# Kernel optimization log

Measured on AMD Instinct MI355X. Metric: run time of the kernel, lower is better.

Reference implementation:

```python
import jax, jax.numpy as jnp
import numpy as np

B, M_IN, N_OUT = 131072, 64, 64


def setup_inputs() -> dict:
    key = jax.random.key(0)
    k1, k2, k3 = jax.random.split(key, 3)
    x = jax.random.normal(k1, (B, M_IN, 4), dtype=jnp.float32)
    x = x.at[:, :, 0].set(0.0)  # pure quaternion input (w-component = 0)
    stdv_w = (2.0 / (M_IN + N_OUT)) ** 0.5
    W_q = jax.random.normal(k2, (N_OUT, M_IN, 4), dtype=jnp.float32) * (stdv_w / 2.0)
    theta_q = jax.random.normal(k3, (N_OUT, 4), dtype=jnp.float32) * 0.01
    theta_q = theta_q.at[:, 0].set(0.0)  # pure quaternion threshold
    return {"x_batch": x, "W_q": W_q, "theta_q": theta_q}


def _hamilton_sum(x, W):
    """s[b,n] = sum_m W[n,m] (x) x[b,m]  (Hamilton product, W on the left).
    x: (B, M, 4), W: (N, M, 4) -> (B, N, 4)"""
    ww, wx, wy, wz = (W[..., i] for i in range(4))   # each (N, M)
    xw, xx, xy, xz = (x[..., i] for i in range(4))   # each (B, M)
    dot = lambda p, q: jnp.einsum('bm,nm->bn', p, q)
    sw = dot(xw, ww) - dot(xx, wx) - dot(xy, wy) - dot(xz, wz)
    sx = dot(xx, ww) + dot(xw, wx) + dot(xz, wy) - dot(xy, wz)
    sy = dot(xy, ww) - dot(xz, wx) + dot(xw, wy) + dot(xx, wz)
    sz = dot(xz, ww) + dot(xy, wx) - dot(xx, wy) + dot(xw, wz)
    return jnp.stack([sw, sx, sy, sz], axis=-1)


def reference(x_batch, W_q, theta_q):
    # Isokawa quaternion neuron: s = sum_m W (x) x - theta; y = sigmoid(s) per component.
    s = _hamilton_sum(x_batch, W_q) - theta_q[None, :, :]  # (B, N, 4) pre-activation (s_internal)
    return jax.nn.sigmoid(s)
```

## Files before the change

### kernel.cpp

```cpp
#include <hip/hip_runtime.h>
#include <hip/hip_bf16.h>


typedef __bf16 bf16_t;
typedef bf16_t bf16x8 __attribute__((ext_vector_type(8)));
typedef bf16_t bf16x4v __attribute__((ext_vector_type(4)));
typedef float f32x4 __attribute__((ext_vector_type(4)));

#define B_TOTAL 131072
#define KDIM 256
#define NDIM 256
#define ROWS 64
#define THREADS 512
#define LDS_STRIDE 264

__global__ void coef_kernel(const float* __restrict__ W, bf16_t* __restrict__ coef) {
    const int widx[4][4] = {{0,1,2,3},{1,0,3,2},{2,3,0,1},{3,2,1,0}};
    const float sgn[4][4] = {{1.f,-1.f,-1.f,-1.f},
                             {1.f, 1.f,-1.f, 1.f},
                             {1.f, 1.f, 1.f,-1.f},
                             {1.f,-1.f, 1.f, 1.f}};
    int F = blockIdx.x * blockDim.x + threadIdx.x;
    int j    = F & 7;
    int lane = (F >> 3) & 63;
    int ks   = (F >> 9) & 7;
    int nt   = F >> 12;
    int col  = nt * 16 + (lane & 15);
    int k    = ks * 32 + (lane >> 4) * 8 + j;
    int n = col >> 2, oc = col & 3;
    int m = k >> 2,   ic = k & 3;
    coef[F] = (bf16_t)(sgn[oc][ic] * W[n * 256 + m * 4 + widx[oc][ic]]);
}

__global__ __launch_bounds__(THREADS, 4)
void main_kernel(const float* __restrict__ x, const bf16x8* __restrict__ coef,
                 const float* __restrict__ theta, float* __restrict__ out) {
    __shared__ __align__(16) bf16_t xs[ROWS * LDS_STRIDE];

    const int tid  = threadIdx.x;
    const int row0 = blockIdx.x * ROWS;
    const int wave = tid >> 6, lane = tid & 63;
    const int l15  = lane & 15, quad = lane >> 4;

    const float4* xp = (const float4*)(x + (long)row0 * KDIM);
    float4 v[8];
#pragma unroll
    for (int i = 0; i < 8; i++) v[i] = xp[tid + THREADS * i];

    bf16x8 breg[2][8];
#pragma unroll
    for (int ct = 0; ct < 2; ct++)
#pragma unroll
        for (int ks = 0; ks < 8; ks++)
            breg[ct][ks] = coef[((wave * 2 + ct) * 8 + ks) * 64 + lane];

#pragma unroll
    for (int i = 0; i < 8; i++) {
        int f = tid + THREADS * i;
        int r = f >> 6;
        int c = (f & 63) * 4;
        bf16x4v w;
        w.x = (bf16_t)v[i].x; w.y = (bf16_t)v[i].y;
        w.z = (bf16_t)v[i].z; w.w = (bf16_t)v[i].w;
        *(bf16x4v*)&xs[r * LDS_STRIDE + c] = w;
    }
    __syncthreads();

    f32x4 acc[4][2];
#pragma unroll
    for (int rt = 0; rt < 4; rt++)
#pragma unroll
        for (int ct = 0; ct < 2; ct++) acc[rt][ct] = (f32x4)(0.f);

#pragma unroll
    for (int ks = 0; ks < 8; ks++) {
        bf16x8 a[4];
#pragma unroll
        for (int rt = 0; rt < 4; rt++)
            a[rt] = *(const bf16x8*)&xs[(rt * 16 + l15) * LDS_STRIDE + ks * 32 + quad * 8];
#pragma unroll
        for (int rt = 0; rt < 4; rt++)
#pragma unroll
            for (int ct = 0; ct < 2; ct++)
                acc[rt][ct] = __builtin_amdgcn_mfma_f32_16x16x32_bf16(
                    a[rt], breg[ct][ks], acc[rt][ct], 0, 0, 0);
    }

    float th[2];
#pragma unroll
    for (int ct = 0; ct < 2; ct++) th[ct] = theta[wave * 32 + ct * 16 + l15];

#pragma unroll
    for (int rt = 0; rt < 4; rt++) {
        int rbase = row0 + rt * 16 + quad * 4;
#pragma unroll
        for (int ct = 0; ct < 2; ct++) {
            int col = wave * 32 + ct * 16 + l15;
#pragma unroll
            for (int r = 0; r < 4; r++) {
                float s = acc[rt][ct][r] - th[ct];
                float y = 1.0f / (1.0f + __expf(-s));
                out[(long)(rbase + r) * NDIM + col] = y;
            }
        }
    }
}

extern "C" void kernel_launch(void* const* d_in, const int* in_sizes, int n_in,
                              void* d_out, int out_size, void* d_ws, size_t ws_size,
                              hipStream_t stream) {
    const float* x     = (const float*)d_in[0];
    const float* W     = (const float*)d_in[1];
    const float* theta = (const float*)d_in[2];
    float* out = (float*)d_out;
    bf16_t* coef = (bf16_t*)d_ws;

    if (ws_size < 65536 * sizeof(bf16_t)) return;

    coef_kernel<<<256, 256, 0, stream>>>(W, coef);
    main_kernel<<<B_TOTAL / ROWS, THREADS, 0, stream>>>(
        x, (const bf16x8*)coef, theta, out);
}
```

Baseline: 243.2 us.

## Process four row tiles per block with prefetched x loads and vectorized stores

Each block now handles four 64-row tiles, so the coefficient registers are loaded once per four tiles, and the next tile's x is loaded from global memory while the current tile is converted and computed. The MFMA operands are swapped so each lane holds four consecutive output columns, which allows 16-byte vector stores of the sigmoid output instead of scalar stores. The reciprocal becomes a fast rcp. The grid shrinks fourfold and launch bounds drop to two blocks per CU, which may reduce parallelism and latency hiding, and the extra register pressure from prefetching is another risk.

```diff
diff --git a/kernel.cpp b/kernel.cpp
--- a/kernel.cpp
+++ b/kernel.cpp
@@ -13,6 +13,8 @@
 #define ROWS 64
 #define THREADS 512
 #define LDS_STRIDE 264
+#define TPB 4
+#define GRID (B_TOTAL / (ROWS * TPB))
 
 __global__ void coef_kernel(const float* __restrict__ W, bf16_t* __restrict__ coef) {
     const int widx[4][4] = {{0,1,2,3},{1,0,3,2},{2,3,0,1},{3,2,1,0}};
@@ -32,20 +34,23 @@
     coef[F] = (bf16_t)(sgn[oc][ic] * W[n * 256 + m * 4 + widx[oc][ic]]);
 }
 
-__global__ __launch_bounds__(THREADS, 4)
+__global__ __launch_bounds__(THREADS, 2)
 void main_kernel(const float* __restrict__ x, const bf16x8* __restrict__ coef,
                  const float* __restrict__ theta, float* __restrict__ out) {
     __shared__ __align__(16) bf16_t xs[ROWS * LDS_STRIDE];
 
     const int tid  = threadIdx.x;
-    const int row0 = blockIdx.x * ROWS;
     const int wave = tid >> 6, lane = tid & 63;
     const int l15  = lane & 15, quad = lane >> 4;
+    const long tile0 = (long)blockIdx.x * TPB;
+    const float4* xbase = (const float4*)x;
 
-    const float4* xp = (const float4*)(x + (long)row0 * KDIM);
     float4 v[8];
+    {
+        const float4* xp = xbase + tile0 * (ROWS * KDIM / 4);
 #pragma unroll
-    for (int i = 0; i < 8; i++) v[i] = xp[tid + THREADS * i];
+        for (int i = 0; i < 8; i++) v[i] = xp[tid + THREADS * i];
+    }
 
     bf16x8 breg[2][8];
 #pragma unroll
@@ -54,53 +59,65 @@
         for (int ks = 0; ks < 8; ks++)
             breg[ct][ks] = coef[((wave * 2 + ct) * 8 + ks) * 64 + lane];
 
+    f32x4 th4[2];
 #pragma unroll
-    for (int i = 0; i < 8; i++) {
-        int f = tid + THREADS * i;
-        int r = f >> 6;
-        int c = (f & 63) * 4;
-        bf16x4v w;
-        w.x = (bf16_t)v[i].x; w.y = (bf16_t)v[i].y;
-        w.z = (bf16_t)v[i].z; w.w = (bf16_t)v[i].w;
-        *(bf16x4v*)&xs[r * LDS_STRIDE + c] = w;
-    }
-    __syncthreads();
-
-    f32x4 acc[4][2];
-#pragma unroll
-    for (int rt = 0; rt < 4; rt++)
-#pragma unroll
-        for (int ct = 0; ct < 2; ct++) acc[rt][ct] = (f32x4)(0.f);
+    for (int ct = 0; ct < 2; ct++)
+        th4[ct] = *(const f32x4*)&theta[wave * 32 + ct * 16 + quad * 4];
 
 #pragma unroll
-    for (int ks = 0; ks < 8; ks++) {
-        bf16x8 a[4];
+    for (int t = 0; t < TPB; t++) {
+        const float4* xq = xbase + (tile0 + t + 1) * (ROWS * KDIM / 4);
 #pragma unroll
-        for (int rt = 0; rt < 4; rt++)
-            a[rt] = *(const bf16x8*)&xs[(rt * 16 + l15) * LDS_STRIDE + ks * 32 + quad * 8];
+        for (int i = 0; i < 8; i++) {
+            int f = tid + THREADS * i;
+            int r = f >> 6;
+            int c = (f & 63) * 4;
+            bf16x4v w;
+            w.x = (bf16_t)v[i].x; w.y = (bf16_t)v[i].y;
+            w.z = (bf16_t)v[i].z; w.w = (bf16_t)v[i].w;
+            *(bf16x4v*)&xs[r * LDS_STRIDE + c] = w;
+            if (t + 1 < TPB) v[i] = xq[tid + THREADS * i];
+        }
+
+        asm volatile("s_waitcnt lgkmcnt(0)" ::: "memory");
+        __builtin_amdgcn_s_barrier();
+
+        f32x4 acc[4][2];
 #pragma unroll
         for (int rt = 0; rt < 4; rt++)
 #pragma unroll
-            for (int ct = 0; ct < 2; ct++)
-                acc[rt][ct] = __builtin_amdgcn_mfma_f32_16x16x32_bf16(
-                    a[rt], breg[ct][ks], acc[rt][ct], 0, 0, 0);
-    }
-
-    float th[2];
-#pragma unroll
-    for (int ct = 0; ct < 2; ct++) th[ct] = theta[wave * 32 + ct * 16 + l15];
+            for (int ct = 0; ct < 2; ct++) acc[rt][ct] = (f32x4)(0.f);
 
 #pragma unroll
-    for (int rt = 0; rt < 4; rt++) {
-        int rbase = row0 + rt * 16 + quad * 4;
+        for (int ks = 0; ks < 8; ks++) {
+            bf16x8 a[4];
 #pragma unroll
-        for (int ct = 0; ct < 2; ct++) {
-            int col = wave * 32 + ct * 16 + l15;
+            for (int rt = 0; rt < 4; rt++)
+                a[rt] = *(const bf16x8*)&xs[(rt * 16 + l15) * LDS_STRIDE + ks * 32 + quad * 8];
 #pragma unroll
-            for (int r = 0; r < 4; r++) {
-                float s = acc[rt][ct][r] - th[ct];
-                float y = 1.0f / (1.0f + __expf(-s));
-                out[(long)(rbase + r) * NDIM + col] = y;
+            for (int rt = 0; rt < 4; rt++)
+#pragma unroll
+                for (int ct = 0; ct < 2; ct++)
+                    acc[rt][ct] = __builtin_amdgcn_mfma_f32_16x16x32_bf16(
+                        breg[ct][ks], a[rt], acc[rt][ct], 0, 0, 0);
+        }
+
+        asm volatile("s_waitcnt lgkmcnt(0)" ::: "memory");
+        __builtin_amdgcn_s_barrier();
+
+        const long row0 = (tile0 + t) * ROWS;
+#pragma unroll
+        for (int rt = 0; rt < 4; rt++) {
+            long row = row0 + rt * 16 + l15;
+#pragma unroll
+            for (int ct = 0; ct < 2; ct++) {
+                f32x4 y;
+#pragma unroll
+                for (int j = 0; j < 4; j++) {
+                    float s = acc[rt][ct][j] - th4[ct][j];
+                    y[j] = __builtin_amdgcn_rcpf(1.0f + __expf(-s));
+                }
+                *(f32x4*)&out[row * NDIM + wave * 32 + ct * 16 + quad * 4] = y;
             }
         }
     }
@@ -118,6 +135,6 @@
     if (ws_size < 65536 * sizeof(bf16_t)) return;
 
     coef_kernel<<<256, 256, 0, stream>>>(W, coef);
-    main_kernel<<<B_TOTAL / ROWS, THREADS, 0, stream>>>(
+    main_kernel<<<GRID, THREADS, 0, stream>>>(
         x, (const bf16x8*)coef, theta, out);
 }
```

Measured after the change: 247.1 us. No clear change (+1.6%).

## Stream x directly into MFMA operands, swap operands for vector stores, persist blocks

Applied to the files above, without the earlier changes.

Removes the LDS staging of x and the block barrier. Each wave now loads fp32 x straight from global memory into bf16 MFMA A-fragments, and each block loops over 16 row tiles, so the coefficient registers are loaded once and reused across 256 rows. Swapping the MFMA operand order puts output columns in the per-lane accumulator elements, which allows float4 stores of the sigmoid result and float4 theta loads. The cost is that all 8 waves of a block read the same x rows redundantly from global/L2, and the grid has fewer blocks to hide latency.

```diff
diff --git a/kernel.cpp b/kernel.cpp
--- a/kernel.cpp
+++ b/kernel.cpp
@@ -4,15 +4,15 @@
 
 typedef __bf16 bf16_t;
 typedef bf16_t bf16x8 __attribute__((ext_vector_type(8)));
-typedef bf16_t bf16x4v __attribute__((ext_vector_type(4)));
 typedef float f32x4 __attribute__((ext_vector_type(4)));
 
 #define B_TOTAL 131072
 #define KDIM 256
 #define NDIM 256
-#define ROWS 64
 #define THREADS 512
-#define LDS_STRIDE 264
+#define ROWS_PER_BLOCK 256
+#define TILES 16
+#define GRID (B_TOTAL / ROWS_PER_BLOCK)
 
 __global__ void coef_kernel(const float* __restrict__ W, bf16_t* __restrict__ coef) {
     const int widx[4][4] = {{0,1,2,3},{1,0,3,2},{2,3,0,1},{3,2,1,0}};
@@ -35,17 +35,9 @@
 __global__ __launch_bounds__(THREADS, 4)
 void main_kernel(const float* __restrict__ x, const bf16x8* __restrict__ coef,
                  const float* __restrict__ theta, float* __restrict__ out) {
-    __shared__ __align__(16) bf16_t xs[ROWS * LDS_STRIDE];
-
     const int tid  = threadIdx.x;
-    const int row0 = blockIdx.x * ROWS;
     const int wave = tid >> 6, lane = tid & 63;
     const int l15  = lane & 15, quad = lane >> 4;
-
-    const float4* xp = (const float4*)(x + (long)row0 * KDIM);
-    float4 v[8];
-#pragma unroll
-    for (int i = 0; i < 8; i++) v[i] = xp[tid + THREADS * i];
 
     bf16x8 breg[2][8];
 #pragma unroll
@@ -54,54 +46,47 @@
         for (int ks = 0; ks < 8; ks++)
             breg[ct][ks] = coef[((wave * 2 + ct) * 8 + ks) * 64 + lane];
 
+    f32x4 th4[2];
 #pragma unroll
-    for (int i = 0; i < 8; i++) {
-        int f = tid + THREADS * i;
-        int r = f >> 6;
-        int c = (f & 63) * 4;
-        bf16x4v w;
-        w.x = (bf16_t)v[i].x; w.y = (bf16_t)v[i].y;
-        w.z = (bf16_t)v[i].z; w.w = (bf16_t)v[i].w;
-        *(bf16x4v*)&xs[r * LDS_STRIDE + c] = w;
-    }
-    __syncthreads();
+    for (int ct = 0; ct < 2; ct++)
+        th4[ct] = *(const f32x4*)&theta[wave * 32 + ct * 16 + quad * 4];
 
-    f32x4 acc[4][2];
-#pragma unroll
-    for (int rt = 0; rt < 4; rt++)
-#pragma unroll
-        for (int ct = 0; ct < 2; ct++) acc[rt][ct] = (f32x4)(0.f);
+    const long row_base = (long)blockIdx.x * ROWS_PER_BLOCK;
+
+#pragma unroll 1
+    for (int t = 0; t < TILES; t++) {
+        const long row = row_base + t * 16 + l15;
+        const float* xr = x + row * KDIM + quad * 8;
+
+        f32x4 acc[2];
+        acc[0] = (f32x4)(0.f);
+        acc[1] = (f32x4)(0.f);
 
 #pragma unroll
-    for (int ks = 0; ks < 8; ks++) {
-        bf16x8 a[4];
-#pragma unroll
-        for (int rt = 0; rt < 4; rt++)
-            a[rt] = *(const bf16x8*)&xs[(rt * 16 + l15) * LDS_STRIDE + ks * 32 + quad * 8];
-#pragma unroll
-        for (int rt = 0; rt < 4; rt++)
-#pragma unroll
-            for (int ct = 0; ct < 2; ct++)
-                acc[rt][ct] = __builtin_amdgcn_mfma_f32_16x16x32_bf16(
-                    a[rt], breg[ct][ks], acc[rt][ct], 0, 0, 0);
-    }
+        for (int ks = 0; ks < 8; ks++) {
+            f32x4 lo = *(const f32x4*)(xr + ks * 32);
+            f32x4 hi = *(const f32x4*)(xr + ks * 32 + 4);
+            bf16x8 af;
+            af[0] = (bf16_t)lo[0]; af[1] = (bf16_t)lo[1];
+            af[2] = (bf16_t)lo[2]; af[3] = (bf16_t)lo[3];
+            af[4] = (bf16_t)hi[0]; af[5] = (bf16_t)hi[1];
+            af[6] = (bf16_t)hi[2]; af[7] = (bf16_t)hi[3];
+            acc[0] = __builtin_amdgcn_mfma_f32_16x16x32_bf16(
+                breg[0][ks], af, acc[0], 0, 0, 0);
+            acc[1] = __builtin_amdgcn_mfma_f32_16x16x32_bf16(
+                breg[1][ks], af, acc[1], 0, 0, 0);
+        }
 
-    float th[2];
-#pragma unroll
-    for (int ct = 0; ct < 2; ct++) th[ct] = theta[wave * 32 + ct * 16 + l15];
-
-#pragma unroll
-    for (int rt = 0; rt < 4; rt++) {
-        int rbase = row0 + rt * 16 + quad * 4;
+        float* orow = out + row * NDIM + wave * 32 + quad * 4;
 #pragma unroll
         for (int ct = 0; ct < 2; ct++) {
-            int col = wave * 32 + ct * 16 + l15;
+            f32x4 y;
 #pragma unroll
-            for (int r = 0; r < 4; r++) {
-                float s = acc[rt][ct][r] - th[ct];
-                float y = 1.0f / (1.0f + __expf(-s));
-                out[(long)(rbase + r) * NDIM + col] = y;
+            for (int j = 0; j < 4; j++) {
+                float s = acc[ct][j] - th4[ct][j];
+                y[j] = __builtin_amdgcn_rcpf(1.0f + __expf(-s));
             }
+            *(f32x4*)(orow + ct * 16) = y;
         }
     }
 }
@@ -118,6 +103,6 @@
     if (ws_size < 65536 * sizeof(bf16_t)) return;
 
     coef_kernel<<<256, 256, 0, stream>>>(W, coef);
-    main_kernel<<<B_TOTAL / ROWS, THREADS, 0, stream>>>(
+    main_kernel<<<GRID, THREADS, 0, stream>>>(
         x, (const bf16x8*)coef, theta, out);
 }
```

Result: slower. 299.7 us (+23.2%).
